# Optimization experiments

Measured on AMD Instinct MI355X. Metric: run time of the kernel, lower is better.

## Reference

```python
import jax, jax.numpy as jnp
import numpy as np

N = 50000
E = 800000
IN_CH = 256
OUT_CH = 64   # per-head channels (PyG out_channels)
HEADS = 4
NEG_SLOPE = 0.2


def setup_inputs() -> dict:
    key = jax.random.key(0)
    k = jax.random.split(key, 8)
    x = jax.random.normal(k[0], (N, IN_CH), dtype=jnp.float32)
    edge_index = jax.random.randint(k[1], (2, E), 0, N, dtype=jnp.int64)
    # GATConv parameters
    W = jax.random.normal(k[2], (IN_CH, HEADS * OUT_CH), dtype=jnp.float32) * (1.0 / np.sqrt(IN_CH))
    att_src = jax.random.normal(k[3], (HEADS, OUT_CH), dtype=jnp.float32) * 0.1
    att_dst = jax.random.normal(k[4], (HEADS, OUT_CH), dtype=jnp.float32) * 0.1
    bias = jnp.zeros((OUT_CH,), dtype=jnp.float32)
    # residual linear (bias=False)
    W_res = jax.random.normal(k[5], (IN_CH, OUT_CH), dtype=jnp.float32) * (1.0 / np.sqrt(IN_CH))
    return {"x": x, "edge_index": edge_index, "W": W, "att_src": att_src,
            "att_dst": att_dst, "bias": bias, "W_res": W_res}


def _gat_forward(x, edge_index, W, att_src, att_dst, bias, W_res):
    # residual branch
    x_res = x @ W_res                                   # [N, OUT_CH]

    # node transform: [N, H, C]
    xw = (x @ W).reshape(N, HEADS, OUT_CH)
    # per-node attention logits, [N, H]
    a_src = jnp.einsum('nhc,hc->nh', xw, att_src)
    a_dst = jnp.einsum('nhc,hc->nh', xw, att_dst)

    # add self-loops (PyG GATConv default add_self_loops=True)
    loops = jnp.arange(N, dtype=edge_index.dtype)
    src = jnp.concatenate([edge_index[0], loops])       # [E+N]
    dst = jnp.concatenate([edge_index[1], loops])       # [E+N]

    # per-edge logits + leaky relu, [E+N, H]
    alpha = jax.nn.leaky_relu(a_src[src] + a_dst[dst], NEG_SLOPE)

    # segment softmax over destination nodes
    m = jax.ops.segment_max(alpha, dst, num_segments=N)    # [N, H]
    e = jnp.exp(alpha - m[dst])
    denom = jax.ops.segment_sum(e, dst, num_segments=N)    # [N, H]
    a = e / denom[dst]                                     # [E+N, H]
    # (dropout p=0.1 on attention coeffs is identity in eval mode)

    # weighted scatter-aggregate: [N, H, C]
    msgs = xw[src] * a[:, :, None]
    out = jax.ops.segment_sum(msgs, dst, num_segments=N)

    # concat=False -> mean over heads, then bias
    x_conv = out.mean(axis=1) + bias                     # [N, OUT_CH]
    return jax.nn.relu(x_conv + x_res)


def reference(x, edge_index, W, att_src, att_dst, bias, W_res):
    return _gat_forward(x, edge_index, W, att_src, att_dst, bias, W_res)
```

## Files before the change

kernel.cpp:

```cpp
#include <hip/hip_runtime.h>
#include <math.h>

#define N_NODES 50000
#define N_EDGES 800000
#define IN_CH   256
#define OUT_CH  64
#define HEADS   4
#define NEG_SLOPE 0.2f
#define NCOLS   320
#define NTILES  20
#define NKK     8
#define PACK_BLOCKS 40
#define GEMM_BLOCKS 782
#define SCAT_BLOCKS 3125

typedef __attribute__((ext_vector_type(8))) short short8;
typedef __attribute__((ext_vector_type(4))) float f32x4;

__device__ __forceinline__ float lrelu(float v) {
    return v > 0.f ? v : NEG_SLOPE * v;
}
__device__ __forceinline__ unsigned bf16_rne(float f) {
    unsigned u = __float_as_uint(f);
    return (u + 0x7FFFu + ((u >> 16) & 1u)) >> 16;
}
__device__ __forceinline__ unsigned pack2(float lo, float hi) {
    return bf16_rne(lo) | (bf16_rne(hi) << 16);
}
__device__ __forceinline__ float bflo(unsigned u) { return __uint_as_float(u << 16); }
__device__ __forceinline__ float bfhi(unsigned u) { return __uint_as_float(u & 0xFFFF0000u); }
__device__ __forceinline__ short8 as_short8(uint4 u) {
    union { uint4 u4; short8 s8; } cv; cv.u4 = u; return cv.s8;
}

__global__ __launch_bounds__(256) void prep(
    const float* __restrict__ W, const float* __restrict__ Wres,
    uint4* __restrict__ Bp, const int* __restrict__ ei,
    int* __restrict__ cnt, int* __restrict__ fill)
{
    if (blockIdx.x < PACK_BLOCKS) {
        const int idx  = blockIdx.x * 256 + threadIdx.x;
        const int kk   = idx / (NTILES * 64);
        const int rem  = idx - kk * (NTILES * 64);
        const int t    = rem >> 6;
        const int lane = rem & 63;
        const int colL = lane & 15, quad = lane >> 4;
        const int col  = t * 16 + colL;
        const int k0   = kk * 32 + quad * 8;
        float v[8];
        #pragma unroll
        for (int j = 0; j < 8; ++j) {
            const int k = k0 + j;
            v[j] = (col < IN_CH) ? W[(size_t)k * IN_CH + col]
                                 : Wres[(size_t)k * OUT_CH + (col - IN_CH)];
        }
        uint4 u;
        u.x = pack2(v[0], v[1]); u.y = pack2(v[2], v[3]);
        u.z = pack2(v[4], v[5]); u.w = pack2(v[6], v[7]);
        Bp[(kk * NTILES + t) * 64 + lane] = u;
    } else {
        const int e = (blockIdx.x - PACK_BLOCKS) * 256 + threadIdx.x;
        if (e < N_NODES) fill[e] = 0;
        if (e < N_EDGES) atomicAdd(&cnt[ei[N_EDGES + e]], 1);
    }
}

__global__ __launch_bounds__(256) void scan_local(
    const int* __restrict__ cnt, int* __restrict__ lscan, int* __restrict__ bsum)
{
    __shared__ int ws[4];
    const int t = threadIdx.x, lane = t & 63, w = t >> 6;
    const int i = blockIdx.x * 256 + t;
    const int v = (i < N_NODES) ? cnt[i] : 0;
    int sc = v;
    #pragma unroll
    for (int off = 1; off < 64; off <<= 1) {
        const int n = __shfl_up(sc, off);
        if (lane >= off) sc += n;
    }
    if (lane == 63) ws[w] = sc;
    __syncthreads();
    int prefix = 0;
    for (int j = 0; j < w; ++j) prefix += ws[j];
    if (i < N_NODES) lscan[i] = prefix + sc - v;
    if (t == 255) bsum[blockIdx.x] = prefix + sc;
}

__global__ __launch_bounds__(256) void scan_bsum(
    const int* __restrict__ bsum, int* __restrict__ bsumx, int nblk)
{
    __shared__ int ws[4];
    const int t = threadIdx.x, lane = t & 63, w = t >> 6;
    const int v = (t < nblk) ? bsum[t] : 0;
    int sc = v;
    #pragma unroll
    for (int off = 1; off < 64; off <<= 1) {
        const int n = __shfl_up(sc, off);
        if (lane >= off) sc += n;
    }
    if (lane == 63) ws[w] = sc;
    __syncthreads();
    int prefix = 0;
    for (int j = 0; j < w; ++j) prefix += ws[j];
    if (t < nblk) bsumx[t] = prefix + sc - v;
}

__global__ __launch_bounds__(256) void gemm_scatter(
    const float* __restrict__ x, const uint4* __restrict__ Bp,
    const float* __restrict__ attS, const float* __restrict__ attD,
    uint2* __restrict__ xw2, float* __restrict__ xres,
    float* __restrict__ asrc, float* __restrict__ adst,
    const int* __restrict__ ei, const int* __restrict__ lscan,
    const int* __restrict__ bsumx, int* __restrict__ fill,
    int* __restrict__ esrc)
{
    __shared__ uint4 Alds[4 * NKK * 64];
    __shared__ float partS[4][4][64];
    __shared__ float partD[4][4][64];

    if (blockIdx.x >= GEMM_BLOCKS) {
        const int e = (blockIdx.x - GEMM_BLOCKS) * 256 + threadIdx.x;
        if (e < N_EDGES) {
            const int d = ei[N_EDGES + e];
            const int pos = atomicAdd(&fill[d], 1);
            esrc[lscan[d] + bsumx[d >> 8] + pos] = ei[e];
        }
        return;
    }

    const int tid = threadIdx.x;
    const int n0  = blockIdx.x * 64;

    #pragma unroll
    for (int i = 0; i < 8; ++i) {
        const int e    = i * 256 + tid;
        const int g    = e >> 9;
        const int kk   = (e >> 6) & 7;
        const int lane = e & 63;
        const int cL   = lane & 15, qd = lane >> 4;
        const int row  = n0 + g * 16 + cL;
        const int k0   = kk * 32 + qd * 8;
        uint4 u = make_uint4(0u, 0u, 0u, 0u);
        if (row < N_NODES) {
            const float4 a = *reinterpret_cast<const float4*>(x + (size_t)row * IN_CH + k0);
            const float4 b = *reinterpret_cast<const float4*>(x + (size_t)row * IN_CH + k0 + 4);
            u.x = pack2(a.x, a.y); u.y = pack2(a.z, a.w);
            u.z = pack2(b.x, b.y); u.w = pack2(b.z, b.w);
        }
        Alds[(g * NKK + kk) * 64 + lane] = u;
    }
    __syncthreads();

    const int lane = tid & 63;
    const int wv   = tid >> 6;
    const int colL = lane & 15, quad = lane >> 4;

    f32x4 acc[4][5];
    #pragma unroll
    for (int rg = 0; rg < 4; ++rg)
        #pragma unroll
        for (int j = 0; j < 5; ++j) acc[rg][j] = (f32x4){0.f, 0.f, 0.f, 0.f};

    for (int kk = 0; kk < NKK; ++kk) {
        uint4 bu[5];
        #pragma unroll
        for (int j = 0; j < 5; ++j)
            bu[j] = Bp[(kk * NTILES + j * 4 + wv) * 64 + lane];
        #pragma unroll
        for (int rg = 0; rg < 4; ++rg) {
            const short8 a = as_short8(Alds[(rg * NKK + kk) * 64 + lane]);
            #pragma unroll
            for (int j = 0; j < 5; ++j)
                acc[rg][j] = __builtin_amdgcn_mfma_f32_16x16x32_bf16(
                    a, as_short8(bu[j]), acc[rg][j], 0, 0, 0);
        }
    }

    #pragma unroll
    for (int h = 0; h < HEADS; ++h) {
        const float aSv = attS[h * 64 + wv * 16 + colL];
        const float aDv = attD[h * 64 + wv * 16 + colL];
        #pragma unroll
        for (int rg = 0; rg < 4; ++rg) {
            #pragma unroll
            for (int r = 0; r < 4; ++r) {
                float vs = acc[rg][h][r] * aSv;
                float vd = acc[rg][h][r] * aDv;
                #pragma unroll
                for (int off = 8; off >= 1; off >>= 1) {
                    vs += __shfl_xor(vs, off);
                    vd += __shfl_xor(vd, off);
                }
                if (colL == 0) {
                    partS[wv][h][rg * 16 + quad * 4 + r] = vs;
                    partD[wv][h][rg * 16 + quad * 4 + r] = vd;
                }
            }
        }
    }
    __syncthreads();
    {
        const int rowIB = tid & 63, h = tid >> 6;
        const int row = n0 + rowIB;
        if (row < N_NODES) {
            const float vs = partS[0][h][rowIB] + partS[1][h][rowIB]
                           + partS[2][h][rowIB] + partS[3][h][rowIB];
            const float vd = partD[0][h][rowIB] + partD[1][h][rowIB]
                           + partD[2][h][rowIB] + partD[3][h][rowIB];
            asrc[row * HEADS + h] = vs;
            adst[row * HEADS + h] = vd;
        }
    }

    #pragma unroll
    for (int rg = 0; rg < 4; ++rg) {
        #pragma unroll
        for (int r = 0; r < 4; ++r) {
            const int row = n0 + rg * 16 + quad * 4 + r;
            if (row < N_NODES) {
                xw2[(size_t)row * 64 + wv * 16 + colL] = make_uint2(
                    pack2(acc[rg][0][r], acc[rg][1][r]),
                    pack2(acc[rg][2][r], acc[rg][3][r]));
                xres[(size_t)row * OUT_CH + wv * 16 + colL] = acc[rg][4][r];
            }
        }
    }
}

__global__ __launch_bounds__(256) void aggregate(
    const int* __restrict__ esrc, const int* __restrict__ lscan,
    const int* __restrict__ bsumx, const int* __restrict__ cnt,
    const float* __restrict__ asrc, const float* __restrict__ adst,
    const uint2* __restrict__ xw2, const float* __restrict__ xres,
    const float* __restrict__ bias, float* __restrict__ out)
{
    __shared__ float4 wbuf[4][64];
    __shared__ int    sbuf[4][64];
    const int lane = threadIdx.x & 63;
    const int wv   = threadIdx.x >> 6;
    const int d = blockIdx.x * 4 + wv;
    if (d >= N_NODES) return;
    const int row = lscan[d] + bsumx[d >> 8];
    const int deg = cnt[d];
    const float4 ad = *reinterpret_cast<const float4*>(adst + (size_t)d * 4);
    const char* xwB = (const char*)xw2;
    const int laneB = lane << 3;

    float dn0 = 0.f, dn1 = 0.f, dn2 = 0.f, dn3 = 0.f;
    float ac0 = 0.f, ac1 = 0.f, ac2 = 0.f, ac3 = 0.f;

    for (int base = 0; base < deg; base += 64) {
        const int m = min(64, deg - base);
        if (lane < m) {
            const int s = esrc[row + base + lane];
            const float4 as = *reinterpret_cast<const float4*>(asrc + (size_t)s * 4);
            const float e0 = __expf(lrelu(as.x + ad.x));
            const float e1 = __expf(lrelu(as.y + ad.y));
            const float e2 = __expf(lrelu(as.z + ad.z));
            const float e3 = __expf(lrelu(as.w + ad.w));
            dn0 += e0; dn1 += e1; dn2 += e2; dn3 += e3;
            wbuf[wv][lane] = make_float4(e0, e1, e2, e3);
            sbuf[wv][lane] = s << 9;
        }
        int j = 0;
        for (; j + 4 <= m; j += 4) {
            uint2 v0 = *(const uint2*)(xwB + sbuf[wv][j]     + laneB);
            uint2 v1 = *(const uint2*)(xwB + sbuf[wv][j + 1] + laneB);
            uint2 v2 = *(const uint2*)(xwB + sbuf[wv][j + 2] + laneB);
            uint2 v3 = *(const uint2*)(xwB + sbuf[wv][j + 3] + laneB);
            {
                const float4 w = wbuf[wv][j];
                ac0 = fmaf(w.x, bflo(v0.x), ac0); ac1 = fmaf(w.y, bfhi(v0.x), ac1);
                ac2 = fmaf(w.z, bflo(v0.y), ac2); ac3 = fmaf(w.w, bfhi(v0.y), ac3);
            }
            {
                const float4 w = wbuf[wv][j + 1];
                ac0 = fmaf(w.x, bflo(v1.x), ac0); ac1 = fmaf(w.y, bfhi(v1.x), ac1);
                ac2 = fmaf(w.z, bflo(v1.y), ac2); ac3 = fmaf(w.w, bfhi(v1.y), ac3);
            }
            {
                const float4 w = wbuf[wv][j + 2];
                ac0 = fmaf(w.x, bflo(v2.x), ac0); ac1 = fmaf(w.y, bfhi(v2.x), ac1);
                ac2 = fmaf(w.z, bflo(v2.y), ac2); ac3 = fmaf(w.w, bfhi(v2.y), ac3);
            }
            {
                const float4 w = wbuf[wv][j + 3];
                ac0 = fmaf(w.x, bflo(v3.x), ac0); ac1 = fmaf(w.y, bfhi(v3.x), ac1);
                ac2 = fmaf(w.z, bflo(v3.y), ac2); ac3 = fmaf(w.w, bfhi(v3.y), ac3);
            }
        }
        for (; j < m; ++j) {
            const float4 w = wbuf[wv][j];
            const uint2 v = *(const uint2*)(xwB + sbuf[wv][j] + laneB);
            ac0 = fmaf(w.x, bflo(v.x), ac0);
            ac1 = fmaf(w.y, bfhi(v.x), ac1);
            ac2 = fmaf(w.z, bflo(v.y), ac2);
            ac3 = fmaf(w.w, bfhi(v.y), ac3);
        }
    }

    #pragma unroll
    for (int off = 32; off >= 1; off >>= 1) {
        dn0 += __shfl_xor(dn0, off);
        dn1 += __shfl_xor(dn1, off);
        dn2 += __shfl_xor(dn2, off);
        dn3 += __shfl_xor(dn3, off);
    }
    const float4 asd = *reinterpret_cast<const float4*>(asrc + (size_t)d * 4);
    const float s0 = __expf(lrelu(asd.x + ad.x));
    const float s1 = __expf(lrelu(asd.y + ad.y));
    const float s2 = __expf(lrelu(asd.z + ad.z));
    const float s3 = __expf(lrelu(asd.w + ad.w));
    const uint2 u = xw2[(size_t)d * 64 + lane];
    ac0 = fmaf(s0, bflo(u.x), ac0); ac1 = fmaf(s1, bfhi(u.x), ac1);
    ac2 = fmaf(s2, bflo(u.y), ac2); ac3 = fmaf(s3, bfhi(u.y), ac3);
    const float i0 = 0.25f / (dn0 + s0);
    const float i1 = 0.25f / (dn1 + s1);
    const float i2 = 0.25f / (dn2 + s2);
    const float i3 = 0.25f / (dn3 + s3);
    const float v = ac0 * i0 + ac1 * i1 + ac2 * i2 + ac3 * i3
                  + bias[lane] + xres[(size_t)d * OUT_CH + lane];
    out[(size_t)d * OUT_CH + lane] = fmaxf(v, 0.f);
}

extern "C" void kernel_launch(void* const* d_in, const int* in_sizes, int n_in,
                              void* d_out, int out_size, void* d_ws, size_t ws_size,
                              hipStream_t stream) {
    const float* x    = (const float*)d_in[0];
    const int*   ei   = (const int*)d_in[1];
    const float* W    = (const float*)d_in[2];
    const float* attS = (const float*)d_in[3];
    const float* attD = (const float*)d_in[4];
    const float* bias = (const float*)d_in[5];
    const float* Wres = (const float*)d_in[6];
    float* out = (float*)d_out;

    char* p = (char*)d_ws;
    uint4*    Bp    = (uint4*)p;    p += (size_t)NKK * NTILES * 64 * 16;
    uint2*    xw2   = (uint2*)p;    p += (size_t)N_NODES * 64 * 8;
    float*    xres  = (float*)p;    p += (size_t)N_NODES * OUT_CH * 4;
    float*    asrc  = (float*)p;    p += (size_t)N_NODES * HEADS * 4;
    float*    adst  = (float*)p;    p += (size_t)N_NODES * HEADS * 4;
    int*      cnt   = (int*)p;      p += (size_t)N_NODES * 4;
    int*      fill  = (int*)p;      p += (size_t)N_NODES * 4;
    int*      lscan = (int*)p;      p += (size_t)N_NODES * 4;
    int*      bsum  = (int*)p;      p += 256 * 4;
    int*      bsumx = (int*)p;      p += 256 * 4;
    int*      esrc  = (int*)p;      p += (size_t)N_EDGES * 4;

    const int nblk_scan = (N_NODES + 255) / 256;

    hipMemsetAsync(cnt, 0, (size_t)N_NODES * sizeof(int), stream);

    prep<<<PACK_BLOCKS + (N_EDGES + 255) / 256, 256, 0, stream>>>(
        W, Wres, Bp, ei, cnt, fill);
    scan_local<<<nblk_scan, 256, 0, stream>>>(cnt, lscan, bsum);
    scan_bsum<<<1, 256, 0, stream>>>(bsum, bsumx, nblk_scan);
    gemm_scatter<<<GEMM_BLOCKS + SCAT_BLOCKS, 256, 0, stream>>>(
        x, Bp, attS, attD, xw2, xres, asrc, adst,
        ei, lscan, bsumx, fill, esrc);
    aggregate<<<(N_NODES + 3) / 4, 256, 0, stream>>>(
        esrc, lscan, bsumx, cnt, asrc, adst, xw2, xres, bias, out);
}
```

Measured before the change: 263.7 us.

## Fold scan into GEMM launch and move attention logits into scatter kernel

The local prefix scan now runs as extra blocks inside the GEMM launch. Each scatter and aggregate block redundantly rescans the 196 block sums in shared memory, which removes the separate scan_local and scan_bsum launches and the serial dependency between them. The per-node attention logits move out of the GEMM epilogue into a new wave-per-node pass in the scatter launch. That pass rereads the bf16 xw, trading extra memory traffic and slightly lower logit precision for a lighter GEMM epilogue and fewer kernel boundaries.

```diff
diff --git a/kernel.cpp b/kernel.cpp
--- a/kernel.cpp
+++ b/kernel.cpp
@@ -12,7 +12,9 @@
 #define NKK     8
 #define PACK_BLOCKS 40
 #define GEMM_BLOCKS 782
+#define SCAN_BLOCKS 196
 #define SCAT_BLOCKS 3125
+#define LOGIT_BLOCKS 12500
 
 typedef __attribute__((ext_vector_type(8))) short short8;
 typedef __attribute__((ext_vector_type(4))) float f32x4;
@@ -65,66 +67,32 @@
     }
 }
 
-__global__ __launch_bounds__(256) void scan_local(
-    const int* __restrict__ cnt, int* __restrict__ lscan, int* __restrict__ bsum)
-{
-    __shared__ int ws[4];
-    const int t = threadIdx.x, lane = t & 63, w = t >> 6;
-    const int i = blockIdx.x * 256 + t;
-    const int v = (i < N_NODES) ? cnt[i] : 0;
-    int sc = v;
-    #pragma unroll
-    for (int off = 1; off < 64; off <<= 1) {
-        const int n = __shfl_up(sc, off);
-        if (lane >= off) sc += n;
-    }
-    if (lane == 63) ws[w] = sc;
-    __syncthreads();
-    int prefix = 0;
-    for (int j = 0; j < w; ++j) prefix += ws[j];
-    if (i < N_NODES) lscan[i] = prefix + sc - v;
-    if (t == 255) bsum[blockIdx.x] = prefix + sc;
-}
-
-__global__ __launch_bounds__(256) void scan_bsum(
-    const int* __restrict__ bsum, int* __restrict__ bsumx, int nblk)
-{
-    __shared__ int ws[4];
-    const int t = threadIdx.x, lane = t & 63, w = t >> 6;
-    const int v = (t < nblk) ? bsum[t] : 0;
-    int sc = v;
-    #pragma unroll
-    for (int off = 1; off < 64; off <<= 1) {
-        const int n = __shfl_up(sc, off);
-        if (lane >= off) sc += n;
-    }
-    if (lane == 63) ws[w] = sc;
-    __syncthreads();
-    int prefix = 0;
-    for (int j = 0; j < w; ++j) prefix += ws[j];
-    if (t < nblk) bsumx[t] = prefix + sc - v;
-}
-
-__global__ __launch_bounds__(256) void gemm_scatter(
+__global__ __launch_bounds__(256) void gemm_scan(
     const float* __restrict__ x, const uint4* __restrict__ Bp,
-    const float* __restrict__ attS, const float* __restrict__ attD,
     uint2* __restrict__ xw2, float* __restrict__ xres,
-    float* __restrict__ asrc, float* __restrict__ adst,
-    const int* __restrict__ ei, const int* __restrict__ lscan,
-    const int* __restrict__ bsumx, int* __restrict__ fill,
-    int* __restrict__ esrc)
+    const int* __restrict__ cnt, int* __restrict__ lscan,
+    int* __restrict__ bsum)
 {
     __shared__ uint4 Alds[4 * NKK * 64];
-    __shared__ float partS[4][4][64];
-    __shared__ float partD[4][4][64];
+    __shared__ int ws[4];
 
     if (blockIdx.x >= GEMM_BLOCKS) {
-        const int e = (blockIdx.x - GEMM_BLOCKS) * 256 + threadIdx.x;
-        if (e < N_EDGES) {
-            const int d = ei[N_EDGES + e];
-            const int pos = atomicAdd(&fill[d], 1);
-            esrc[lscan[d] + bsumx[d >> 8] + pos] = ei[e];
-        }
+        const int bid = blockIdx.x - GEMM_BLOCKS;
+        const int t = threadIdx.x, lane = t & 63, w = t >> 6;
+        const int i = bid * 256 + t;
+        const int v = (i < N_NODES) ? cnt[i] : 0;
+        int sc = v;
+        #pragma unroll
+        for (int off = 1; off < 64; off <<= 1) {
+            const int n = __shfl_up(sc, off);
+            if (lane >= off) sc += n;
+        }
+        if (lane == 63) ws[w] = sc;
+        __syncthreads();
+        int prefix = 0;
+        for (int j = 0; j < w; ++j) prefix += ws[j];
+        if (i < N_NODES) lscan[i] = prefix + sc - v;
+        if (t == 255) bsum[bid] = prefix + sc;
         return;
     }
 
@@ -177,42 +145,6 @@
     }
 
     #pragma unroll
-    for (int h = 0; h < HEADS; ++h) {
-        const float aSv = attS[h * 64 + wv * 16 + colL];
-        const float aDv = attD[h * 64 + wv * 16 + colL];
-        #pragma unroll
-        for (int rg = 0; rg < 4; ++rg) {
-            #pragma unroll
-            for (int r = 0; r < 4; ++r) {
-                float vs = acc[rg][h][r] * aSv;
-                float vd = acc[rg][h][r] * aDv;
-                #pragma unroll
-                for (int off = 8; off >= 1; off >>= 1) {
-                    vs += __shfl_xor(vs, off);
-                    vd += __shfl_xor(vd, off);
-                }
-                if (colL == 0) {
-                    partS[wv][h][rg * 16 + quad * 4 + r] = vs;
-                    partD[wv][h][rg * 16 + quad * 4 + r] = vd;
-                }
-            }
-        }
-    }
-    __syncthreads();
-    {
-        const int rowIB = tid & 63, h = tid >> 6;
-        const int row = n0 + rowIB;
-        if (row < N_NODES) {
-            const float vs = partS[0][h][rowIB] + partS[1][h][rowIB]
-                           + partS[2][h][rowIB] + partS[3][h][rowIB];
-            const float vd = partD[0][h][rowIB] + partD[1][h][rowIB]
-                           + partD[2][h][rowIB] + partD[3][h][rowIB];
-            asrc[row * HEADS + h] = vs;
-            adst[row * HEADS + h] = vd;
-        }
-    }
-
-    #pragma unroll
     for (int rg = 0; rg < 4; ++rg) {
         #pragma unroll
         for (int r = 0; r < 4; ++r) {
@@ -227,20 +159,96 @@
     }
 }
 
+__global__ __launch_bounds__(256) void scatter_logits(
+    const int* __restrict__ ei, const int* __restrict__ lscan,
+    const int* __restrict__ bsum, int* __restrict__ fill,
+    int* __restrict__ esrc,
+    const uint2* __restrict__ xw2, const float* __restrict__ attS,
+    const float* __restrict__ attD, float* __restrict__ asrc,
+    float* __restrict__ adst)
+{
+    const int t = threadIdx.x;
+    const int lane = t & 63, wv = t >> 6;
+
+    if (blockIdx.x < SCAT_BLOCKS) {
+        __shared__ int bsx[256];
+        __shared__ int ws[4];
+        const int v = (t < SCAN_BLOCKS) ? bsum[t] : 0;
+        int sc = v;
+        #pragma unroll
+        for (int off = 1; off < 64; off <<= 1) {
+            const int n = __shfl_up(sc, off);
+            if (lane >= off) sc += n;
+        }
+        if (lane == 63) ws[wv] = sc;
+        __syncthreads();
+        int prefix = 0;
+        for (int j = 0; j < wv; ++j) prefix += ws[j];
+        bsx[t] = prefix + sc - v;
+        __syncthreads();
+
+        const int e = blockIdx.x * 256 + t;
+        if (e < N_EDGES) {
+            const int d = ei[N_EDGES + e];
+            const int pos = atomicAdd(&fill[d], 1);
+            esrc[lscan[d] + bsx[d >> 8] + pos] = ei[e];
+        }
+        return;
+    }
+
+    const int n = (blockIdx.x - SCAT_BLOCKS) * 4 + wv;
+    const uint2 v = xw2[(size_t)n * 64 + lane];
+    const float h0 = bflo(v.x), h1 = bfhi(v.x), h2 = bflo(v.y), h3 = bfhi(v.y);
+    float s0 = h0 * attS[lane],       s1 = h1 * attS[64 + lane];
+    float s2 = h2 * attS[128 + lane], s3 = h3 * attS[192 + lane];
+    float d0 = h0 * attD[lane],       d1 = h1 * attD[64 + lane];
+    float d2 = h2 * attD[128 + lane], d3 = h3 * attD[192 + lane];
+    #pragma unroll
+    for (int off = 32; off >= 1; off >>= 1) {
+        s0 += __shfl_xor(s0, off); s1 += __shfl_xor(s1, off);
+        s2 += __shfl_xor(s2, off); s3 += __shfl_xor(s3, off);
+        d0 += __shfl_xor(d0, off); d1 += __shfl_xor(d1, off);
+        d2 += __shfl_xor(d2, off); d3 += __shfl_xor(d3, off);
+    }
+    if (lane == 0)
+        *reinterpret_cast<float4*>(asrc + (size_t)n * 4) = make_float4(s0, s1, s2, s3);
+    if (lane == 1)
+        *reinterpret_cast<float4*>(adst + (size_t)n * 4) = make_float4(d0, d1, d2, d3);
+}
+
 __global__ __launch_bounds__(256) void aggregate(
     const int* __restrict__ esrc, const int* __restrict__ lscan,
-    const int* __restrict__ bsumx, const int* __restrict__ cnt,
+    const int* __restrict__ bsum, const int* __restrict__ cnt,
     const float* __restrict__ asrc, const float* __restrict__ adst,
     const uint2* __restrict__ xw2, const float* __restrict__ xres,
     const float* __restrict__ bias, float* __restrict__ out)
 {
     __shared__ float4 wbuf[4][64];
     __shared__ int    sbuf[4][64];
-    const int lane = threadIdx.x & 63;
-    const int wv   = threadIdx.x >> 6;
+    __shared__ int    bsx[256];
+    __shared__ int    ws[4];
+    const int t = threadIdx.x;
+    const int lane = t & 63;
+    const int wv   = t >> 6;
+
+    {
+        const int v = (t < SCAN_BLOCKS) ? bsum[t] : 0;
+        int sc = v;
+        #pragma unroll
+        for (int off = 1; off < 64; off <<= 1) {
+            const int n = __shfl_up(sc, off);
+            if (lane >= off) sc += n;
+        }
+        if (lane == 63) ws[wv] = sc;
+        __syncthreads();
+        int prefix = 0;
+        for (int j = 0; j < wv; ++j) prefix += ws[j];
+        bsx[t] = prefix + sc - v;
+        __syncthreads();
+    }
+
     const int d = blockIdx.x * 4 + wv;
-    if (d >= N_NODES) return;
-    const int row = lscan[d] + bsumx[d >> 8];
+    const int row = lscan[d] + bsx[d >> 8];
     const int deg = cnt[d];
     const float4 ad = *reinterpret_cast<const float4*>(adst + (size_t)d * 4);
     const char* xwB = (const char*)xw2;
@@ -345,20 +353,16 @@
     int*      fill  = (int*)p;      p += (size_t)N_NODES * 4;
     int*      lscan = (int*)p;      p += (size_t)N_NODES * 4;
     int*      bsum  = (int*)p;      p += 256 * 4;
-    int*      bsumx = (int*)p;      p += 256 * 4;
     int*      esrc  = (int*)p;      p += (size_t)N_EDGES * 4;
-
-    const int nblk_scan = (N_NODES + 255) / 256;
 
     hipMemsetAsync(cnt, 0, (size_t)N_NODES * sizeof(int), stream);
 
     prep<<<PACK_BLOCKS + (N_EDGES + 255) / 256, 256, 0, stream>>>(
         W, Wres, Bp, ei, cnt, fill);
-    scan_local<<<nblk_scan, 256, 0, stream>>>(cnt, lscan, bsum);
-    scan_bsum<<<1, 256, 0, stream>>>(bsum, bsumx, nblk_scan);
-    gemm_scatter<<<GEMM_BLOCKS + SCAT_BLOCKS, 256, 0, stream>>>(
-        x, Bp, attS, attD, xw2, xres, asrc, adst,
-        ei, lscan, bsumx, fill, esrc);
-    aggregate<<<(N_NODES + 3) / 4, 256, 0, stream>>>(
-        esrc, lscan, bsumx, cnt, asrc, adst, xw2, xres, bias, out);
-}
+    gemm_scan<<<GEMM_BLOCKS + SCAN_BLOCKS, 256, 0, stream>>>(
+        x, Bp, xw2, xres, cnt, lscan, bsum);
+    scatter_logits<<<SCAT_BLOCKS + LOGIT_BLOCKS, 256, 0, stream>>>(
+        ei, lscan, bsum, fill, esrc, xw2, attS, attD, asrc, adst);
+    aggregate<<<LOGIT_BLOCKS, 256, 0, stream>>>(
+        esrc, lscan, bsum, cnt, asrc, adst, xw2, xres, bias, out);
+}
```

New measurement: 294.0 us. 1.11x slower.
